# Performance work log

Measured on AMD Instinct MI355X. Metric: run time of the kernel, lower is better.

The kernel has to match this reference:

```python
import jax, jax.numpy as jnp
import numpy as np

C = 256          # channels
K_SIZE = 3       # involution kernel size
GROUPS = 16      # groups g
HIDDEN = C // 4  # reduction_ratio = 4
B, H, W = 8, 64, 64


def setup_inputs() -> dict:
    key = jax.random.key(0)
    k0, k1, k2 = jax.random.split(key, 3)
    kk = K_SIZE * K_SIZE
    return {
        "x": jax.random.normal(k0, (B, C, H, W), dtype=jnp.float32),
        # 1x1 conv weights stored as matrices [out_ch, in_ch]
        "w_reduce": jax.random.normal(k1, (HIDDEN, C), dtype=jnp.float32) * 0.05,
        "b_reduce": jnp.zeros((HIDDEN,), dtype=jnp.float32),
        "w_span": jax.random.normal(k2, (GROUPS * kk, HIDDEN), dtype=jnp.float32) * 0.05,
        "b_span": jnp.zeros((GROUPS * kk,), dtype=jnp.float32),
    }


def reference(x, w_reduce, b_reduce, w_span, b_span):
    b, c, h, w = x.shape
    k, g = K_SIZE, GROUPS
    kk = k * k
    # stride == 1 -> sigma is identity; kernel generator: 1x1 conv -> relu -> 1x1 conv
    hid = jax.nn.relu(jnp.einsum('oc,bcxy->boxy', w_reduce, x)
                      + b_reduce[None, :, None, None])
    Kmap = (jnp.einsum('oc,bcxy->boxy', w_span, hid)
            + b_span[None, :, None, None])            # [B, g*kk, H, W]
    Kmap = Kmap.reshape(b, g, kk, h, w)
    # unfold with padding k//2, stride 1: extract k*k shifted views
    pad = k // 2
    xp = jnp.pad(x, ((0, 0), (0, 0), (pad, pad), (pad, pad)))
    patches = jnp.stack(
        [xp[:, :, i:i + h, j:j + w] for i in range(k) for j in range(k)],
        axis=2)                                        # [B, C, kk, H, W]
    patches = patches.reshape(b, g, c // g, kk, h, w)
    # location-specific, channel-agnostic multiply-reduce over kk
    out = jnp.einsum('bgnkhw,bgkhw->bgnhw', patches, Kmap)
    return out.reshape(b, c, h, w)
```

## Files before the change

### kernel.cpp

```cpp
#include <hip/hip_runtime.h>

#define CCH 256
#define HIDN 64
#define NB  8
#define NHW 4096

#define W1PK_OFF 0
#define W2PK_OFF 16384

typedef __attribute__((ext_vector_type(8))) short bf16x8;
typedef __attribute__((ext_vector_type(4))) float f32x4;
typedef __attribute__((ext_vector_type(4))) int   i32x4;
typedef __attribute__((ext_vector_type(2))) int   i32x2;

__device__ __forceinline__ unsigned short bf16_rne(float f) {
    unsigned u = __float_as_uint(f);
    u += 0x7FFFu + ((u >> 16) & 1u);
    return (unsigned short)(u >> 16);
}
__device__ __forceinline__ float bf16_f32(unsigned short s) {
    return __uint_as_float(((unsigned)s) << 16);
}
__device__ __forceinline__ bf16x8 as_bf16(i32x4 v) {
    union { i32x4 i; bf16x8 b; } u; u.i = v; return u.b;
}

__global__ __launch_bounds__(256) void prepack_kernel(
    const float* __restrict__ w_reduce, const float* __restrict__ w_span,
    unsigned* __restrict__ ws)
{
    const int idx = blockIdx.x * 256 + threadIdx.x;
    int d, lane, pass, ks, mt, K, base;
    const float* W;
    if (idx < 16384) {
        d = idx & 3; lane = (idx >> 2) & 63; pass = (idx >> 8) & 1;
        ks = (idx >> 9) & 7; mt = (idx >> 12) & 3;
        W = w_reduce; K = 256; base = W1PK_OFF + idx;
    } else {
        const int i2 = idx - 16384;
        d = i2 & 3; lane = (i2 >> 2) & 63; pass = (i2 >> 8) & 1;
        ks = (i2 >> 9) & 1; mt = i2 >> 10;
        W = w_span; K = 64; base = W2PK_OFF + i2;
    }
    const int m = mt * 16 + (lane & 15);
    const int g = (lane >> 4) & 3;
    unsigned o = 0;
    #pragma unroll
    for (int h = 0; h < 2; ++h) {
        const int ei = d * 2 + h;
        const int k  = ks * 32 + ((ei >> 2) << 4) + (g << 2) + (ei & 3);
        const float w = W[m * K + k];
        const unsigned short hi = bf16_rne(w);
        const unsigned short v  = pass ? bf16_rne(w - bf16_f32(hi)) : hi;
        o |= ((unsigned)v) << (16 * h);
    }
    ws[base] = o;
}

__global__ __launch_bounds__(512, 4) void invol_fused(
    const float* __restrict__ x,
    const float* __restrict__ b_reduce,
    const float* __restrict__ b_span,
    const unsigned* __restrict__ wpk,
    float* __restrict__ out)
{
    __shared__ __align__(16) int lds[8576];
    short* const lds_s = (short*)lds;

    const int tid  = threadIdx.x;
    const int lane = tid & 63;
    const int wid  = __builtin_amdgcn_readfirstlane(tid >> 6);
    const int n    = lane & 15;
    const int g    = lane >> 4;

    const int raw = blockIdx.x;
    const int row = ((raw & 7) << 6) | (raw >> 3);
    const int b   = row >> 6;
    const int hr  = row & 63;

    const float* xb = x + (size_t)b * (CCH * NHW) + hr * 64;

    {
        const int px = tid & 63;
        const int c0 = (tid >> 6) * 32;
        const float* xp = xb + (size_t)c0 * NHW + px;
        int* dst = &lds[px * 134 + (c0 >> 1)];
        #pragma unroll
        for (int i = 0; i < 16; ++i) {
            const float f0 = xp[(2 * i) * NHW];
            const float f1 = xp[(2 * i + 1) * NHW];
            dst[i] = (int)((unsigned)bf16_rne(f0) |
                           ((unsigned)bf16_rne(f1) << 16));
        }
    }
    __syncthreads();

    const int ot  = wid >> 1;
    const int pt0 = (wid & 1) * 2;
    f32x4 acc0 = {0.f, 0.f, 0.f, 0.f};
    f32x4 acc1 = {0.f, 0.f, 0.f, 0.f};
    const int* w1pk = (const int*)wpk + W1PK_OFF;

    #pragma unroll
    for (int ks = 0; ks < 8; ++ks) {
        const int abase = ot * 4096 + ks * 512 + lane * 4;
        const i32x4 ah = *(const i32x4*)(w1pk + abase);
        const i32x4 al = *(const i32x4*)(w1pk + abase + 256);
        const int bb0 = (pt0 * 16 + n) * 134 + ks * 16 + g * 2;
        const int bb1 = bb0 + 16 * 134;
        const i32x2 p0 = *(const i32x2*)&lds[bb0];
        const i32x2 p1 = *(const i32x2*)&lds[bb0 + 8];
        const i32x2 q0 = *(const i32x2*)&lds[bb1];
        const i32x2 q1 = *(const i32x2*)&lds[bb1 + 8];
        const i32x4 b0 = {p0.x, p0.y, p1.x, p1.y};
        const i32x4 b1 = {q0.x, q0.y, q1.x, q1.y};
        const bf16x8 fa_h = as_bf16(ah), fa_l = as_bf16(al);
        const bf16x8 fb0 = as_bf16(b0), fb1 = as_bf16(b1);
        acc0 = __builtin_amdgcn_mfma_f32_16x16x32_bf16(fa_h, fb0, acc0, 0, 0, 0);
        acc0 = __builtin_amdgcn_mfma_f32_16x16x32_bf16(fa_l, fb0, acc0, 0, 0, 0);
        acc1 = __builtin_amdgcn_mfma_f32_16x16x32_bf16(fa_h, fb1, acc1, 0, 0, 0);
        acc1 = __builtin_amdgcn_mfma_f32_16x16x32_bf16(fa_l, fb1, acc1, 0, 0, 0);
    }
    __syncthreads();

    {
        const f32x4 br = *(const f32x4*)&b_reduce[ot * 16 + g * 4];
        const unsigned h00 = (unsigned)bf16_rne(fmaxf(acc0.x + br.x, 0.f))
                           | ((unsigned)bf16_rne(fmaxf(acc0.y + br.y, 0.f)) << 16);
        const unsigned h01 = (unsigned)bf16_rne(fmaxf(acc0.z + br.z, 0.f))
                           | ((unsigned)bf16_rne(fmaxf(acc0.w + br.w, 0.f)) << 16);
        const unsigned h10 = (unsigned)bf16_rne(fmaxf(acc1.x + br.x, 0.f))
                           | ((unsigned)bf16_rne(fmaxf(acc1.y + br.y, 0.f)) << 16);
        const unsigned h11 = (unsigned)bf16_rne(fmaxf(acc1.z + br.z, 0.f))
                           | ((unsigned)bf16_rne(fmaxf(acc1.w + br.w, 0.f)) << 16);
        const i32x2 w0 = {(int)h00, (int)h01};
        const i32x2 w1 = {(int)h10, (int)h11};
        *(i32x2*)&lds[(pt0 * 16 + n) * 38 + ot * 8 + g * 2]       = w0;
        *(i32x2*)&lds[((pt0 + 1) * 16 + n) * 38 + ot * 8 + g * 2] = w1;
    }
    __syncthreads();

    const int* w2pk = (const int*)wpk + W2PK_OFF;
    for (int t = wid; t < 36; t += 8) {
        const int jt = t >> 2, pt = t & 3;
        f32x4 acc = {0.f, 0.f, 0.f, 0.f};
        #pragma unroll
        for (int ks = 0; ks < 2; ++ks) {
            const int abase = jt * 1024 + ks * 512 + lane * 4;
            const i32x4 ah = *(const i32x4*)(w2pk + abase);
            const i32x4 al = *(const i32x4*)(w2pk + abase + 256);
            const int bb = (pt * 16 + n) * 38 + ks * 16 + g * 2;
            const i32x2 p0 = *(const i32x2*)&lds[bb];
            const i32x2 p1 = *(const i32x2*)&lds[bb + 8];
            const i32x4 bi = {p0.x, p0.y, p1.x, p1.y};
            const bf16x8 fb = as_bf16(bi);
            acc = __builtin_amdgcn_mfma_f32_16x16x32_bf16(as_bf16(ah), fb, acc, 0, 0, 0);
            acc = __builtin_amdgcn_mfma_f32_16x16x32_bf16(as_bf16(al), fb, acc, 0, 0, 0);
        }
        const f32x4 bs = *(const f32x4*)&b_span[jt * 16 + g * 4];
        const int jb = jt * 16 + g * 4;
        const int pxi = pt * 16 + n;
        lds_s[4864 + (jb + 0) * 66 + pxi] = (short)bf16_rne(acc.x + bs.x);
        lds_s[4864 + (jb + 1) * 66 + pxi] = (short)bf16_rne(acc.y + bs.y);
        lds_s[4864 + (jb + 2) * 66 + pxi] = (short)bf16_rne(acc.z + bs.z);
        lds_s[4864 + (jb + 3) * 66 + pxi] = (short)bf16_rne(acc.w + bs.w);
    }
    __syncthreads();

    const bool vwm = (lane > 0), vwp = (lane < 63);
    const bool vhm = (hr  > 0), vhp = (hr  < 63);
    const bool vk[9] = { vhm && vwm, vhm, vhm && vwp,
                         vwm,        true, vwp,
                         vhp && vwm, vhp, vhp && vwp };
    float kv[18];
    #pragma unroll
    for (int jj = 0; jj < 18; ++jj) {
        const float v = bf16_f32((unsigned short)
                        lds_s[4864 + (wid * 18 + jj) * 66 + lane]);
        kv[jj] = vk[jj % 9] ? v : 0.f;
    }
    const int oWm = vwm ? -1  : 0, oWp = vwp ? 1  : 0;
    const int oHm = vhm ? -64 : 0, oHp = vhp ? 64 : 0;
    const int oo[9] = { oHm + oWm, oHm, oHm + oWp,
                        oWm,       0,   oWp,
                        oHp + oWm, oHp, oHp + oWp };

    const float* xrow = xb + lane;
    float*       orow = out + (size_t)b * (CCH * NHW) + hr * 64 + lane;

    #pragma unroll
    for (int m = 0; m < 32; ++m) {
        const int c  = wid * 32 + m;
        const int gl = m >> 4;
        const float* xc = xrow + (size_t)c * NHW;
        float a = 0.f;
        #pragma unroll
        for (int k = 0; k < 9; ++k)
            a = fmaf(xc[oo[k]], kv[gl * 9 + k], a);
        orow[(size_t)c * NHW] = a;
    }
}

extern "C" void kernel_launch(void* const* d_in, const int* in_sizes, int n_in,
                              void* d_out, int out_size, void* d_ws, size_t ws_size,
                              hipStream_t stream) {
    const float* x        = (const float*)d_in[0];
    const float* w_reduce = (const float*)d_in[1];
    const float* b_reduce = (const float*)d_in[2];
    const float* w_span   = (const float*)d_in[3];
    const float* b_span   = (const float*)d_in[4];
    float* out = (float*)d_out;
    unsigned* ws = (unsigned*)d_ws;

    prepack_kernel<<<dim3(100), dim3(256), 0, stream>>>(w_reduce, w_span, ws);
    invol_fused<<<dim3(NB * 64), dim3(512), 0, stream>>>(
        x, b_reduce, b_span, ws, out);
}
```

Baseline: 104.7 us.

## Split each image row across two blocks to double grid size and occupancy

Each block now handles half of an image row (32 pixels) instead of a full row, which doubles the grid to 1024 blocks. LDS shrinks, and the hidden and kernel-map buffers are laid out in separate regions, so one barrier can be dropped. Launch bounds rise to 6 waves per SIMD. Per-block work is halved (one MFMA tile per wave), and the epilogue maps 16 groups onto half-waves. The aim is to fill the GPU better than 512 blocks did, at the cost of loading the packed weights twice as often and using 32-lane halves with shorter contiguous x accesses.

```diff
diff --git a/kernel.cpp b/kernel.cpp
--- a/kernel.cpp
+++ b/kernel.cpp
@@ -57,14 +57,14 @@
     ws[base] = o;
 }
 
-__global__ __launch_bounds__(512, 4) void invol_fused(
+__global__ __launch_bounds__(512, 6) void invol_fused(
     const float* __restrict__ x,
     const float* __restrict__ b_reduce,
     const float* __restrict__ b_span,
     const unsigned* __restrict__ wpk,
     float* __restrict__ out)
 {
-    __shared__ __align__(16) int lds[8576];
+    __shared__ __align__(16) int lds[7952];
     short* const lds_s = (short*)lds;
 
     const int tid  = threadIdx.x;
@@ -74,31 +74,37 @@
     const int g    = lane >> 4;
 
     const int raw = blockIdx.x;
-    const int row = ((raw & 7) << 6) | (raw >> 3);
-    const int b   = row >> 6;
-    const int hr  = row & 63;
-
-    const float* xb = x + (size_t)b * (CCH * NHW) + hr * 64;
+    const int id  = ((raw & 7) << 7) | (raw >> 3);
+    const int b   = id >> 7;
+    const int hr  = (id >> 1) & 63;
+    const int ph  = id & 1;
+
+    const float* xb = x + (size_t)b * (CCH * NHW) + hr * 64 + ph * 32;
 
     {
-        const int px = tid & 63;
-        const int c0 = (tid >> 6) * 32;
+        const int px = tid & 31;
+        const int c0 = (tid >> 5) * 16;
         const float* xp = xb + (size_t)c0 * NHW + px;
         int* dst = &lds[px * 134 + (c0 >> 1)];
-        #pragma unroll
-        for (int i = 0; i < 16; ++i) {
+        int tmp[8];
+        #pragma unroll
+        for (int i = 0; i < 8; ++i) {
             const float f0 = xp[(2 * i) * NHW];
             const float f1 = xp[(2 * i + 1) * NHW];
-            dst[i] = (int)((unsigned)bf16_rne(f0) |
+            tmp[i] = (int)((unsigned)bf16_rne(f0) |
                            ((unsigned)bf16_rne(f1) << 16));
         }
+        #pragma unroll
+        for (int i = 0; i < 4; ++i) {
+            const i32x2 v = {tmp[2 * i], tmp[2 * i + 1]};
+            *(i32x2*)&dst[2 * i] = v;
+        }
     }
     __syncthreads();
 
-    const int ot  = wid >> 1;
-    const int pt0 = (wid & 1) * 2;
-    f32x4 acc0 = {0.f, 0.f, 0.f, 0.f};
-    f32x4 acc1 = {0.f, 0.f, 0.f, 0.f};
+    const int ot = wid >> 1;
+    const int pt = wid & 1;
+    f32x4 acc = {0.f, 0.f, 0.f, 0.f};
     const int* w1pk = (const int*)wpk + W1PK_OFF;
 
     #pragma unroll
@@ -106,78 +112,68 @@
         const int abase = ot * 4096 + ks * 512 + lane * 4;
         const i32x4 ah = *(const i32x4*)(w1pk + abase);
         const i32x4 al = *(const i32x4*)(w1pk + abase + 256);
-        const int bb0 = (pt0 * 16 + n) * 134 + ks * 16 + g * 2;
-        const int bb1 = bb0 + 16 * 134;
-        const i32x2 p0 = *(const i32x2*)&lds[bb0];
-        const i32x2 p1 = *(const i32x2*)&lds[bb0 + 8];
-        const i32x2 q0 = *(const i32x2*)&lds[bb1];
-        const i32x2 q1 = *(const i32x2*)&lds[bb1 + 8];
+        const int bb = (pt * 16 + n) * 134 + ks * 16 + g * 2;
+        const i32x2 p0 = *(const i32x2*)&lds[bb];
+        const i32x2 p1 = *(const i32x2*)&lds[bb + 8];
         const i32x4 b0 = {p0.x, p0.y, p1.x, p1.y};
-        const i32x4 b1 = {q0.x, q0.y, q1.x, q1.y};
-        const bf16x8 fa_h = as_bf16(ah), fa_l = as_bf16(al);
-        const bf16x8 fb0 = as_bf16(b0), fb1 = as_bf16(b1);
-        acc0 = __builtin_amdgcn_mfma_f32_16x16x32_bf16(fa_h, fb0, acc0, 0, 0, 0);
-        acc0 = __builtin_amdgcn_mfma_f32_16x16x32_bf16(fa_l, fb0, acc0, 0, 0, 0);
-        acc1 = __builtin_amdgcn_mfma_f32_16x16x32_bf16(fa_h, fb1, acc1, 0, 0, 0);
-        acc1 = __builtin_amdgcn_mfma_f32_16x16x32_bf16(fa_l, fb1, acc1, 0, 0, 0);
-    }
-    __syncthreads();
+        const bf16x8 fb = as_bf16(b0);
+        acc = __builtin_amdgcn_mfma_f32_16x16x32_bf16(as_bf16(ah), fb, acc, 0, 0, 0);
+        acc = __builtin_amdgcn_mfma_f32_16x16x32_bf16(as_bf16(al), fb, acc, 0, 0, 0);
+    }
 
     {
         const f32x4 br = *(const f32x4*)&b_reduce[ot * 16 + g * 4];
-        const unsigned h00 = (unsigned)bf16_rne(fmaxf(acc0.x + br.x, 0.f))
-                           | ((unsigned)bf16_rne(fmaxf(acc0.y + br.y, 0.f)) << 16);
-        const unsigned h01 = (unsigned)bf16_rne(fmaxf(acc0.z + br.z, 0.f))
-                           | ((unsigned)bf16_rne(fmaxf(acc0.w + br.w, 0.f)) << 16);
-        const unsigned h10 = (unsigned)bf16_rne(fmaxf(acc1.x + br.x, 0.f))
-                           | ((unsigned)bf16_rne(fmaxf(acc1.y + br.y, 0.f)) << 16);
-        const unsigned h11 = (unsigned)bf16_rne(fmaxf(acc1.z + br.z, 0.f))
-                           | ((unsigned)bf16_rne(fmaxf(acc1.w + br.w, 0.f)) << 16);
-        const i32x2 w0 = {(int)h00, (int)h01};
-        const i32x2 w1 = {(int)h10, (int)h11};
-        *(i32x2*)&lds[(pt0 * 16 + n) * 38 + ot * 8 + g * 2]       = w0;
-        *(i32x2*)&lds[((pt0 + 1) * 16 + n) * 38 + ot * 8 + g * 2] = w1;
+        const unsigned h0 = (unsigned)bf16_rne(fmaxf(acc.x + br.x, 0.f))
+                          | ((unsigned)bf16_rne(fmaxf(acc.y + br.y, 0.f)) << 16);
+        const unsigned h1 = (unsigned)bf16_rne(fmaxf(acc.z + br.z, 0.f))
+                          | ((unsigned)bf16_rne(fmaxf(acc.w + br.w, 0.f)) << 16);
+        const i32x2 hv = {(int)h0, (int)h1};
+        *(i32x2*)&lds[4288 + (pt * 16 + n) * 38 + ot * 8 + g * 2] = hv;
     }
     __syncthreads();
 
     const int* w2pk = (const int*)wpk + W2PK_OFF;
-    for (int t = wid; t < 36; t += 8) {
-        const int jt = t >> 2, pt = t & 3;
-        f32x4 acc = {0.f, 0.f, 0.f, 0.f};
+    for (int t = wid; t < 18; t += 8) {
+        const int jt = t >> 1, pt2 = t & 1;
+        f32x4 a2 = {0.f, 0.f, 0.f, 0.f};
         #pragma unroll
         for (int ks = 0; ks < 2; ++ks) {
             const int abase = jt * 1024 + ks * 512 + lane * 4;
             const i32x4 ah = *(const i32x4*)(w2pk + abase);
             const i32x4 al = *(const i32x4*)(w2pk + abase + 256);
-            const int bb = (pt * 16 + n) * 38 + ks * 16 + g * 2;
+            const int bb = 4288 + (pt2 * 16 + n) * 38 + ks * 16 + g * 2;
             const i32x2 p0 = *(const i32x2*)&lds[bb];
             const i32x2 p1 = *(const i32x2*)&lds[bb + 8];
             const i32x4 bi = {p0.x, p0.y, p1.x, p1.y};
             const bf16x8 fb = as_bf16(bi);
-            acc = __builtin_amdgcn_mfma_f32_16x16x32_bf16(as_bf16(ah), fb, acc, 0, 0, 0);
-            acc = __builtin_amdgcn_mfma_f32_16x16x32_bf16(as_bf16(al), fb, acc, 0, 0, 0);
+            a2 = __builtin_amdgcn_mfma_f32_16x16x32_bf16(as_bf16(ah), fb, a2, 0, 0, 0);
+            a2 = __builtin_amdgcn_mfma_f32_16x16x32_bf16(as_bf16(al), fb, a2, 0, 0, 0);
         }
         const f32x4 bs = *(const f32x4*)&b_span[jt * 16 + g * 4];
         const int jb = jt * 16 + g * 4;
-        const int pxi = pt * 16 + n;
-        lds_s[4864 + (jb + 0) * 66 + pxi] = (short)bf16_rne(acc.x + bs.x);
-        lds_s[4864 + (jb + 1) * 66 + pxi] = (short)bf16_rne(acc.y + bs.y);
-        lds_s[4864 + (jb + 2) * 66 + pxi] = (short)bf16_rne(acc.z + bs.z);
-        lds_s[4864 + (jb + 3) * 66 + pxi] = (short)bf16_rne(acc.w + bs.w);
+        const int pxi = pt2 * 16 + n;
+        lds_s[11008 + (jb + 0) * 34 + pxi] = (short)bf16_rne(a2.x + bs.x);
+        lds_s[11008 + (jb + 1) * 34 + pxi] = (short)bf16_rne(a2.y + bs.y);
+        lds_s[11008 + (jb + 2) * 34 + pxi] = (short)bf16_rne(a2.z + bs.z);
+        lds_s[11008 + (jb + 3) * 34 + pxi] = (short)bf16_rne(a2.w + bs.w);
     }
     __syncthreads();
 
-    const bool vwm = (lane > 0), vwp = (lane < 63);
-    const bool vhm = (hr  > 0), vhp = (hr  < 63);
+    const int px  = lane & 31;
+    const int grp = wid * 2 + (lane >> 5);
+    const int w   = ph * 32 + px;
+
+    const bool vwm = (w > 0), vwp = (w < 63);
+    const bool vhm = (hr > 0), vhp = (hr < 63);
     const bool vk[9] = { vhm && vwm, vhm, vhm && vwp,
                          vwm,        true, vwp,
                          vhp && vwm, vhp, vhp && vwp };
-    float kv[18];
-    #pragma unroll
-    for (int jj = 0; jj < 18; ++jj) {
+    float kv[9];
+    #pragma unroll
+    for (int r = 0; r < 9; ++r) {
         const float v = bf16_f32((unsigned short)
-                        lds_s[4864 + (wid * 18 + jj) * 66 + lane]);
-        kv[jj] = vk[jj % 9] ? v : 0.f;
+                        lds_s[11008 + (grp * 9 + r) * 34 + px]);
+        kv[r] = vk[r] ? v : 0.f;
     }
     const int oWm = vwm ? -1  : 0, oWp = vwp ? 1  : 0;
     const int oHm = vhm ? -64 : 0, oHp = vhp ? 64 : 0;
@@ -185,18 +181,17 @@
                         oWm,       0,   oWp,
                         oHp + oWm, oHp, oHp + oWp };
 
-    const float* xrow = xb + lane;
-    float*       orow = out + (size_t)b * (CCH * NHW) + hr * 64 + lane;
-
-    #pragma unroll
-    for (int m = 0; m < 32; ++m) {
-        const int c  = wid * 32 + m;
-        const int gl = m >> 4;
+    const float* xrow = x   + (size_t)b * (CCH * NHW) + hr * 64 + w;
+    float*       orow = out + (size_t)b * (CCH * NHW) + hr * 64 + w;
+
+    #pragma unroll
+    for (int m = 0; m < 16; ++m) {
+        const int c = grp * 16 + m;
         const float* xc = xrow + (size_t)c * NHW;
         float a = 0.f;
         #pragma unroll
         for (int k = 0; k < 9; ++k)
-            a = fmaf(xc[oo[k]], kv[gl * 9 + k], a);
+            a = fmaf(xc[oo[k]], kv[k], a);
         orow[(size_t)c * NHW] = a;
     }
 }
@@ -213,6 +208,6 @@
     unsigned* ws = (unsigned*)d_ws;
 
     prepack_kernel<<<dim3(100), dim3(256), 0, stream>>>(w_reduce, w_span, ws);
-    invol_fused<<<dim3(NB * 64), dim3(512), 0, stream>>>(
+    invol_fused<<<dim3(NB * 128), dim3(512), 0, stream>>>(
         x, b_reduce, b_span, ws, out);
 }
```

Result: no change. 106.1 us (+1.4%).
